# Kernel tuning notes

Measured on AMD Instinct MI355X. Metric: run time of the kernel, lower is better.

Reference implementation:

```python
import jax, jax.numpy as jnp
import numpy as np

B, P, E = 16, 1024, 768
HID, HEADS = 768, 12
DH = HID // HEADS  # 64
EPS = 1e-5


def setup_inputs() -> dict:
    key = jax.random.key(0)
    ks = jax.random.split(key, 4)
    return {
        "x": jax.random.normal(ks[0], (B, P, E), dtype=jnp.float32),
        "ln_weight": jnp.ones((P, E), dtype=jnp.float32),
        "ln_bias": jnp.zeros((P, E), dtype=jnp.float32),
        "qkv": jax.random.normal(ks[1], (E, 3 * HID), dtype=jnp.float32),
        "lin_w": jax.random.normal(ks[2], (HID, E), dtype=jnp.float32) * 0.02,
        "lin_b": jax.random.normal(ks[3], (E,), dtype=jnp.float32) * 0.02,
    }


def reference(x, ln_weight, ln_bias, qkv, lin_w, lin_b):
    # LayerNorm over the last TWO dims (patches, emb), per torch nn.LayerNorm((P, E))
    mean = jnp.mean(x, axis=(-2, -1), keepdims=True)
    var = jnp.var(x, axis=(-2, -1), keepdims=True)
    xn = (x - mean) / jnp.sqrt(var + EPS) * ln_weight + ln_bias

    # QKV projection: [B,P,E] @ [E,3*HID] -> [B,P,3*HID]
    proj = xn @ qkv
    # view(B,P,heads,-1) then permute -> [B,heads,P,3*DH]; chunk along last dim
    proj = proj.reshape(B, P, HEADS, 3 * DH).transpose(0, 2, 1, 3)
    q, k, v = proj[..., :DH], proj[..., DH:2 * DH], proj[..., 2 * DH:]

    # Softmax-free attention: (Q K^T) V
    atten = jnp.einsum("bhqd,bhkd->bhqk", q, k)  # [B,H,P,P]
    out = jnp.einsum("bhqk,bhkd->bhqd", atten, v)  # [B,H,P,DH]

    out = out.transpose(0, 2, 1, 3).reshape(B, P, HID)
    # dropout p=0.0 (eval) -> identity
    out = jax.nn.relu(out @ lin_w + lin_b)
    return out + x
```

## Files before the change

### kernel.cpp

```cpp
#include <hip/hip_runtime.h>
#include <hip/hip_bf16.h>
#include <cstdint>

#define BB   16
#define PP   1024
#define EE   768
#define HID  768
#define NH   12
#define DH   64
#define NPB  (PP * EE)
#define MROWS (BB * PP)

typedef __bf16 bf16_t;
typedef __bf16 bf16x8 __attribute__((ext_vector_type(8)));
typedef float  f32x4  __attribute__((ext_vector_type(4)));

__device__ __forceinline__ void gld16(const void* g, void* l) {
    __builtin_amdgcn_global_load_lds(
        (const __attribute__((address_space(1))) void*)(uintptr_t)g,
        (__attribute__((address_space(3))) void*)(uint32_t)(uintptr_t)l,
        16, 0, 0);
}

__global__ __launch_bounds__(256) void stats1_kernel(const float* __restrict__ x,
                                                     float* __restrict__ part) {
    int bid = blockIdx.x;
    int b = bid >> 6, s = bid & 63;
    const float4* xp = (const float4*)(x + (size_t)b * NPB + (size_t)s * 12288);
    float sum = 0.f, ss = 0.f;
#pragma unroll
    for (int i = 0; i < 12; ++i) {
        float4 v = xp[i * 256 + threadIdx.x];
        sum += v.x + v.y + v.z + v.w;
        ss  += v.x * v.x + v.y * v.y + v.z * v.z + v.w * v.w;
    }
#pragma unroll
    for (int off = 32; off > 0; off >>= 1) {
        sum += __shfl_down(sum, off, 64);
        ss  += __shfl_down(ss,  off, 64);
    }
    __shared__ float tmp[8];
    int wave = threadIdx.x >> 6, lane = threadIdx.x & 63;
    if (lane == 0) { tmp[wave * 2] = sum; tmp[wave * 2 + 1] = ss; }
    __syncthreads();
    if (threadIdx.x == 0) {
        part[bid * 2]     = tmp[0] + tmp[2] + tmp[4] + tmp[6];
        part[bid * 2 + 1] = tmp[1] + tmp[3] + tmp[5] + tmp[7];
    }
}

__global__ __launch_bounds__(256) void prep_kernel(const float* __restrict__ qkvw,
                                                   const float* __restrict__ linw,
                                                   const float* __restrict__ part,
                                                   bf16_t* __restrict__ qkvT,
                                                   bf16_t* __restrict__ lwT,
                                                   float* __restrict__ stats) {
    int bid = blockIdx.x;
    if (bid < 576) {
        __shared__ float lds[64][65];
        const float* src; bf16_t* dst; int r0, c0, W;
        if (bid < 432) {
            int tr = bid / 36, tc = bid - tr * 36;
            r0 = tr * 64; c0 = tc * 64; src = qkvw; W = 2304; dst = qkvT;
        } else {
            int bb = bid - 432;
            int tr = bb / 12, tc = bb - tr * 12;
            r0 = tr * 64; c0 = tc * 64; src = linw; W = 768; dst = lwT;
        }
        int t = threadIdx.x;
        int rr = t >> 4, cc4 = (t & 15) * 4;
#pragma unroll
        for (int j = 0; j < 4; ++j) {
            float4 v = *(const float4*)(src + (size_t)(r0 + rr + j * 16) * W + c0 + cc4);
            lds[rr + j * 16][cc4 + 0] = v.x;
            lds[rr + j * 16][cc4 + 1] = v.y;
            lds[rr + j * 16][cc4 + 2] = v.z;
            lds[rr + j * 16][cc4 + 3] = v.w;
        }
        __syncthreads();
        int cl = t >> 3, rgl = (t & 7) * 8;
#pragma unroll
        for (int jj = 0; jj < 2; ++jj) {
            int c = jj * 32 + cl;
            union { bf16_t h[8]; uint4 u; } o;
#pragma unroll
            for (int k = 0; k < 8; ++k) o.h[k] = (bf16_t)lds[rgl + k][c];
            *(uint4*)(dst + (size_t)(c0 + c) * 768 + r0 + rgl) = o.u;
        }
    } else {
        int wave = threadIdx.x >> 6, lane = threadIdx.x & 63;
#pragma unroll
        for (int j = 0; j < 4; ++j) {
            int b = wave * 4 + j;
            float sum = part[(b * 64 + lane) * 2];
            float ss  = part[(b * 64 + lane) * 2 + 1];
#pragma unroll
            for (int off = 32; off > 0; off >>= 1) {
                sum += __shfl_down(sum, off, 64);
                ss  += __shfl_down(ss,  off, 64);
            }
            if (lane == 0) {
                const float inv_n = 1.f / (float)NPB;
                float mean = sum * inv_n;
                float var  = ss * inv_n - mean * mean;
                stats[b * 2]     = mean;
                stats[b * 2 + 1] = rsqrtf(var + 1e-5f);
            }
        }
    }
}

__global__ __launch_bounds__(256) void ln_apply_kernel(const float* __restrict__ x,
                                                       const float* __restrict__ lnw,
                                                       const float* __restrict__ lnb,
                                                       const float* __restrict__ stats,
                                                       bf16_t* __restrict__ xn) {
    int i = (blockIdx.x * 256 + threadIdx.x) * 8;
    int b = i / NPB;
    int r = i - b * NPB;
    float mean = stats[b * 2], rstd = stats[b * 2 + 1];
    float4 x0 = *(const float4*)(x + i),     x1 = *(const float4*)(x + i + 4);
    float4 w0 = *(const float4*)(lnw + r),   w1 = *(const float4*)(lnw + r + 4);
    float4 c0 = *(const float4*)(lnb + r),   c1 = *(const float4*)(lnb + r + 4);
    union { bf16_t h[8]; uint4 u; } o;
    o.h[0] = (bf16_t)((x0.x - mean) * rstd * w0.x + c0.x);
    o.h[1] = (bf16_t)((x0.y - mean) * rstd * w0.y + c0.y);
    o.h[2] = (bf16_t)((x0.z - mean) * rstd * w0.z + c0.z);
    o.h[3] = (bf16_t)((x0.w - mean) * rstd * w0.w + c0.w);
    o.h[4] = (bf16_t)((x1.x - mean) * rstd * w1.x + c1.x);
    o.h[5] = (bf16_t)((x1.y - mean) * rstd * w1.y + c1.y);
    o.h[6] = (bf16_t)((x1.z - mean) * rstd * w1.z + c1.z);
    o.h[7] = (bf16_t)((x1.w - mean) * rstd * w1.w + c1.w);
    *(uint4*)(xn + i) = o.u;
}

template <int KDIM>
__device__ __forceinline__ void gemm_core_128(const bf16_t* __restrict__ A,
                                              const bf16_t* __restrict__ Bt,
                                              int mBase, int nBase,
                                              f32x4 acc[4][4],
                                              bf16_t* As, bf16_t* Bs) {
    const int t = threadIdx.x;
    const int lane = t & 63, wave = t >> 6;
    const int wm = wave >> 1, wn = wave & 1;
    const int m16 = lane & 15, quad = lane >> 4;

    const int sr = t >> 3, s8 = t & 7;
    const bf16_t* pa[4]; const bf16_t* pb[4];
#pragma unroll
    for (int i = 0; i < 4; ++i) {
        int row = i * 32 + sr;
        int g = (s8 - (row & 7)) & 7;
        pa[i] = A  + (size_t)(mBase + row) * KDIM + g * 8;
        pb[i] = Bt + (size_t)(nBase + row) * KDIM + g * 8;
    }

    int raOff[4][2], rbOff[4][2];
#pragma unroll
    for (int i = 0; i < 4; ++i) {
        int ra = wm * 64 + i * 16 + m16;
        int rb = wn * 64 + i * 16 + m16;
#pragma unroll
        for (int ks = 0; ks < 2; ++ks) {
            raOff[i][ks] = ra * 64 + (((ks * 4 + quad) + (ra & 7)) & 7) * 8;
            rbOff[i][ks] = rb * 64 + (((ks * 4 + quad) + (rb & 7)) & 7) * 8;
        }
    }

    const f32x4 z = {0.f, 0.f, 0.f, 0.f};
#pragma unroll
    for (int mm = 0; mm < 4; ++mm)
#pragma unroll
        for (int nn = 0; nn < 4; ++nn) acc[mm][nn] = z;

    for (int k0 = 0; k0 < KDIM; k0 += 64) {
        __syncthreads();
#pragma unroll
        for (int i = 0; i < 4; ++i) {
            gld16(pa[i] + k0, As + i * 2048 + t * 8);
            gld16(pb[i] + k0, Bs + i * 2048 + t * 8);
        }
        __syncthreads();
#pragma unroll
        for (int ks = 0; ks < 2; ++ks) {
            bf16x8 af[4], bfv[4];
#pragma unroll
            for (int i = 0; i < 4; ++i) {
                af[i]  = *(const bf16x8*)(As + raOff[i][ks]);
                bfv[i] = *(const bf16x8*)(Bs + rbOff[i][ks]);
            }
#pragma unroll
            for (int mm = 0; mm < 4; ++mm)
#pragma unroll
                for (int nn = 0; nn < 4; ++nn)
                    acc[mm][nn] = __builtin_amdgcn_mfma_f32_16x16x32_bf16(
                        af[mm], bfv[nn], acc[mm][nn], 0, 0, 0);
        }
    }
}

__global__ __launch_bounds__(256, 2) void gemm_qkv_kernel(const bf16_t* __restrict__ xn,
                                                          const bf16_t* __restrict__ qkvT,
                                                          bf16_t* __restrict__ q,
                                                          bf16_t* __restrict__ kt,
                                                          bf16_t* __restrict__ vt) {
    __shared__ bf16_t smem[24576];
    const int t = threadIdx.x, lane = t & 63, wave = t >> 6;
    const int wm = wave >> 1, wn = wave & 1;
    const int m16 = lane & 15, quad = lane >> 4;

    const int lb = blockIdx.y * 9 + blockIdx.x;
    const int id = (lb & 7) * 144 + (lb >> 3);
    const int tx = id % 9, ty = id / 9;
    const int mBase = ty * 128, nBase = tx * 256;

    const bf16_t* gsrc[6];
    int ldst[6];
#pragma unroll
    for (int j = 0; j < 2; ++j) {
        int c = t + 256 * j;
        int l = c >> 3, lg = ((c & 7) - (l & 7)) & 7;
        gsrc[j] = xn + (size_t)(mBase + l + (lg >> 2) * 64) * 768 + (lg & 3) * 8;
        ldst[j] = c * 8;
    }
#pragma unroll
    for (int j = 0; j < 4; ++j) {
        int c = t + 256 * j;
        int l = c >> 3, lg = ((c & 7) - (l & 7)) & 7;
        gsrc[2 + j] = qkvT + (size_t)(nBase + l + (lg >> 2) * 128) * 768 + (lg & 3) * 8;
        ldst[2 + j] = 4096 + c * 8;
    }

    int aOff[4], bOff[8];
#pragma unroll
    for (int mf = 0; mf < 4; ++mf)
        aOff[mf] = (mf * 16 + m16) * 64 + (((wm * 4 + quad) + (m16 & 7)) & 7) * 8;
#pragma unroll
    for (int nf = 0; nf < 8; ++nf)
        bOff[nf] = 4096 + (nf * 16 + m16) * 64 + (((wn * 4 + quad) + (m16 & 7)) & 7) * 8;

    f32x4 acc[4][8];
    const f32x4 z = {0.f, 0.f, 0.f, 0.f};
#pragma unroll
    for (int mf = 0; mf < 4; ++mf)
#pragma unroll
        for (int nf = 0; nf < 8; ++nf) acc[mf][nf] = z;

#pragma unroll
    for (int j = 0; j < 6; ++j) gld16(gsrc[j], smem + ldst[j]);
    __syncthreads();

#pragma unroll
    for (int it = 0; it < 12; ++it) {
#pragma unroll
        for (int s = 0; s < 2; ++s) {
            const int step = it * 2 + s;
            const int par = s * 12288, nxt = 12288 - par;
            if (step < 23) {
                const int kq = (step + 1) * 32;
#pragma unroll
                for (int j = 0; j < 6; ++j)
                    gld16(gsrc[j] + kq, smem + nxt + ldst[j]);
            }
            bf16x8 af[4], bf0[4], bf1[4];
#pragma unroll
            for (int mf = 0; mf < 4; ++mf)
                af[mf] = *(const bf16x8*)(smem + par + aOff[mf]);
#pragma unroll
            for (int nf = 0; nf < 4; ++nf)
                bf0[nf] = *(const bf16x8*)(smem + par + bOff[nf]);
            __builtin_amdgcn_s_setprio(1);
#pragma unroll
            for (int mf = 0; mf < 4; ++mf)
#pragma unroll
                for (int nf = 0; nf < 4; ++nf)
                    acc[mf][nf] = __builtin_amdgcn_mfma_f32_16x16x32_bf16(
                        af[mf], bf0[nf], acc[mf][nf], 0, 0, 0);
            __builtin_amdgcn_s_setprio(0);
            __builtin_amdgcn_s_barrier();
#pragma unroll
            for (int nf = 0; nf < 4; ++nf)
                bf1[nf] = *(const bf16x8*)(smem + par + bOff[4 + nf]);
            __builtin_amdgcn_s_setprio(1);
#pragma unroll
            for (int mf = 0; mf < 4; ++mf)
#pragma unroll
                for (int nf = 0; nf < 4; ++nf)
                    acc[mf][4 + nf] = __builtin_amdgcn_mfma_f32_16x16x32_bf16(
                        af[mf], bf1[nf], acc[mf][4 + nf], 0, 0, 0);
            __builtin_amdgcn_s_setprio(0);
            __syncthreads();
        }
    }

    bf16_t* slot = smem + wave * 4608;
    const int b = mBase >> 10, p0 = mBase & 1023;

#pragma unroll
    for (int half = 0; half < 2; ++half) {
        const int g64 = tx * 4 + wn * 2 + half;
        const int cls = g64 % 3, h = g64 / 3;
        if (cls == 0) {
#pragma unroll
            for (int mf = 0; mf < 4; ++mf)
#pragma unroll
                for (int nfl = 0; nfl < 4; ++nfl)
#pragma unroll
                    for (int i = 0; i < 4; ++i)
                        slot[(mf * 16 + quad * 4 + i) * 72 + nfl * 16 + m16] =
                            (bf16_t)acc[mf][half * 4 + nfl][i];
            asm volatile("s_waitcnt lgkmcnt(0)" ::: "memory");
            __builtin_amdgcn_sched_barrier(0);
#pragma unroll
            for (int j = 0; j < 8; ++j) {
                int r = j * 8 + (lane >> 3), cc = lane & 7;
                bf16x8 val = *(const bf16x8*)(slot + r * 72 + cc * 8);
                *(bf16x8*)(q + ((size_t)(b * 1024 + p0 + wm * 64 + r)) * 768 +
                           h * 64 + cc * 8) = val;
            }
        } else {
            bf16_t* dst = (cls == 1) ? kt : vt;
            const size_t bh = (size_t)(b * 12 + h);
#pragma unroll
            for (int mf = 0; mf < 4; ++mf)
#pragma unroll
                for (int nfl = 0; nfl < 4; ++nfl) {
                    int c = nfl * 16 + m16;
                    union { bf16_t hh[4]; uint2 u; } pk;
#pragma unroll
                    for (int i = 0; i < 4; ++i)
                        pk.hh[i] = (bf16_t)acc[mf][half * 4 + nfl][i];
                    *(uint2*)(slot + c * 72 + mf * 16 + quad * 4) = pk.u;
                }
            asm volatile("s_waitcnt lgkmcnt(0)" ::: "memory");
            __builtin_amdgcn_sched_barrier(0);
#pragma unroll
            for (int j = 0; j < 8; ++j) {
                int c = (lane >> 3) + j * 8, r8 = (lane & 7) * 8;
                bf16x8 val = *(const bf16x8*)(slot + c * 72 + r8);
                *(bf16x8*)(dst + (bh * 64 + c) * 1024 + p0 + wm * 64 + r8) = val;
            }
        }
        if (half == 0) {
            asm volatile("s_waitcnt lgkmcnt(0)" ::: "memory");
            __builtin_amdgcn_sched_barrier(0);
        }
    }
}

__global__ __launch_bounds__(256) void kv_kernel(const bf16_t* __restrict__ kt,
                                                 const bf16_t* __restrict__ vt,
                                                 bf16_t* __restrict__ thi,
                                                 bf16_t* __restrict__ tlo) {
    __shared__ float red[4 * 64 * 65];
    const int bh = blockIdx.x;
    const bf16_t* Kb = kt + (size_t)bh * DH * PP;
    const bf16_t* Vb = vt + (size_t)bh * DH * PP;
    const int t = threadIdx.x;
    const int lane = t & 63, wave = t >> 6;
    const int m16 = lane & 15, quad = lane >> 4;
    const f32x4 z = {0.f, 0.f, 0.f, 0.f};
    f32x4 acc[4][4];
#pragma unroll
    for (int mm = 0; mm < 4; ++mm)
#pragma unroll
        for (int nn = 0; nn < 4; ++nn) acc[mm][nn] = z;

    for (int ks = 0; ks < 8; ++ks) {
        int kb = wave * 256 + ks * 32 + quad * 8;
        bf16x8 af[4], bfv[4];
#pragma unroll
        for (int mm = 0; mm < 4; ++mm)
            af[mm] = *(const bf16x8*)(Kb + (size_t)(mm * 16 + m16) * PP + kb);
#pragma unroll
        for (int nn = 0; nn < 4; ++nn)
            bfv[nn] = *(const bf16x8*)(Vb + (size_t)(nn * 16 + m16) * PP + kb);
#pragma unroll
        for (int mm = 0; mm < 4; ++mm)
#pragma unroll
            for (int nn = 0; nn < 4; ++nn)
                acc[mm][nn] = __builtin_amdgcn_mfma_f32_16x16x32_bf16(
                    af[mm], bfv[nn], acc[mm][nn], 0, 0, 0);
    }
#pragma unroll
    for (int mm = 0; mm < 4; ++mm)
#pragma unroll
        for (int nn = 0; nn < 4; ++nn)
#pragma unroll
            for (int i = 0; i < 4; ++i)
                red[wave * 4160 + (mm * 16 + quad * 4 + i) * 65 + nn * 16 + m16] =
                    acc[mm][nn][i];
    __syncthreads();
#pragma unroll
    for (int j = 0; j < 16; ++j) {
        int idx = j * 256 + t;
        int m = idx >> 6, n = idx & 63;
        int a = m * 65 + n;
        float s = red[a] + red[4160 + a] + red[8320 + a] + red[12480 + a];
        bf16_t hi = (bf16_t)s;
        float lo = s - (float)hi;
        thi[(size_t)bh * 4096 + idx] = hi;
        tlo[(size_t)bh * 4096 + idx] = (bf16_t)lo;
    }
}

__global__ __launch_bounds__(256) void u_kernel(const bf16_t* __restrict__ thi,
                                                const bf16_t* __restrict__ tlo,
                                                const bf16_t* __restrict__ lwT,
                                                bf16_t* __restrict__ ut) {
    const int bh = blockIdx.x;
    const int b = bh / NH, h = bh - b * NH;
    const int nBase = blockIdx.y * 256;
    const bf16_t* Th = thi + (size_t)bh * 4096;
    const bf16_t* Tl = tlo + (size_t)bh * 4096;
    const int t = threadIdx.x, lane = t & 63, wave = t >> 6;
    const int wm = wave >> 1, wn = wave & 1;
    const int m16 = lane & 15, quad = lane >> 4;
    const f32x4 z = {0.f, 0.f, 0.f, 0.f};
    f32x4 acc[2][8];
#pragma unroll
    for (int mm = 0; mm < 2; ++mm)
#pragma unroll
        for (int nn = 0; nn < 8; ++nn) acc[mm][nn] = z;

#pragma unroll
    for (int ks = 0; ks < 2; ++ks) {
        bf16x8 ah[2], al[2], bfr[8];
#pragma unroll
        for (int mm = 0; mm < 2; ++mm) {
            ah[mm] = *(const bf16x8*)(Th + (wm * 32 + mm * 16 + m16) * 64 + ks * 32 + quad * 8);
            al[mm] = *(const bf16x8*)(Tl + (wm * 32 + mm * 16 + m16) * 64 + ks * 32 + quad * 8);
        }
#pragma unroll
        for (int nn = 0; nn < 8; ++nn)
            bfr[nn] = *(const bf16x8*)(
                lwT + (size_t)(nBase + wn * 128 + nn * 16 + m16) * 768 + h * 64 + ks * 32 + quad * 8);
#pragma unroll
        for (int mm = 0; mm < 2; ++mm)
#pragma unroll
            for (int nn = 0; nn < 8; ++nn) {
                acc[mm][nn] = __builtin_amdgcn_mfma_f32_16x16x32_bf16(
                    ah[mm], bfr[nn], acc[mm][nn], 0, 0, 0);
                acc[mm][nn] = __builtin_amdgcn_mfma_f32_16x16x32_bf16(
                    al[mm], bfr[nn], acc[mm][nn], 0, 0, 0);
            }
    }
#pragma unroll
    for (int mm = 0; mm < 2; ++mm)
#pragma unroll
        for (int nn = 0; nn < 8; ++nn) {
            int e  = nBase + wn * 128 + nn * 16 + m16;
            int d1 = wm * 32 + mm * 16 + quad * 4;
            union { bf16_t hh[4]; uint2 u; } pk;
#pragma unroll
            for (int i = 0; i < 4; ++i) pk.hh[i] = (bf16_t)acc[mm][nn][i];
            *(uint2*)(ut + ((size_t)b * 768 + e) * 768 + h * 64 + d1) = pk.u;
        }
}

__global__ __launch_bounds__(256) void gemm_out_kernel(const bf16_t* __restrict__ q,
                                                       const bf16_t* __restrict__ ut,
                                                       const float* __restrict__ linb,
                                                       const float* __restrict__ x,
                                                       float* __restrict__ out) {
    __shared__ bf16_t smem[16384];
    f32x4 acc[4][4];
    const int lb  = blockIdx.y * 6 + blockIdx.x;
    const int swz = (lb & 7) * 96 + (lb >> 3);
    const int tx  = swz % 6, ty = swz / 6;
    const int mBase = ty * 128, nBase = tx * 128;
    const int b = mBase >> 10;
    gemm_core_128<768>(q, ut + (size_t)b * 768 * 768, mBase, nBase, acc,
                       smem, smem + 8192);

    const int lane = threadIdx.x & 63, wave = threadIdx.x >> 6;
    const int wm = wave >> 1, wn = wave & 1;
    const int m16 = lane & 15, quad = lane >> 4;
#pragma unroll
    for (int mm = 0; mm < 4; ++mm) {
#pragma unroll
        for (int i = 0; i < 4; ++i) {
            size_t row = mBase + wm * 64 + mm * 16 + quad * 4 + i;
#pragma unroll
            for (int nn = 0; nn < 4; ++nn) {
                int col = nBase + wn * 64 + nn * 16 + m16;
                float v = acc[mm][nn][i] + linb[col];
                v = fmaxf(v, 0.f) + x[row * EE + col];
                out[row * EE + col] = v;
            }
        }
    }
}

extern "C" void kernel_launch(void* const* d_in, const int* in_sizes, int n_in,
                              void* d_out, int out_size, void* d_ws, size_t ws_size,
                              hipStream_t stream) {
    const float* x    = (const float*)d_in[0];
    const float* lnw  = (const float*)d_in[1];
    const float* lnb  = (const float*)d_in[2];
    const float* qkvw = (const float*)d_in[3];
    const float* linw = (const float*)d_in[4];
    const float* linb = (const float*)d_in[5];
    float* out = (float*)d_out;
    char* ws = (char*)d_ws;

    float*  part  = (float*)(ws + 0);
    float*  stats = (float*)(ws + 8192);
    bf16_t* xn    = (bf16_t*)(ws + 8448);
    bf16_t* qkvT  = (bf16_t*)(ws + 25174272);
    bf16_t* lwT   = (bf16_t*)(ws + 28713216);
    bf16_t* q     = (bf16_t*)(ws + 29892864);
    bf16_t* kt    = (bf16_t*)(ws + 55058688);
    bf16_t* vt    = (bf16_t*)(ws + 80224512);
    bf16_t* thi   = qkvT;
    bf16_t* tlo   = qkvT + 192 * 4096;
    bf16_t* ut    = kt;

    stats1_kernel<<<dim3(BB * 64), dim3(256), 0, stream>>>(x, part);
    prep_kernel<<<dim3(577), dim3(256), 0, stream>>>(qkvw, linw, part, qkvT, lwT, stats);
    ln_apply_kernel<<<dim3(6144), dim3(256), 0, stream>>>(x, lnw, lnb, stats, xn);
    gemm_qkv_kernel<<<dim3(9, 128), dim3(256), 0, stream>>>(xn, qkvT, q, kt, vt);
    kv_kernel<<<dim3(192), dim3(256), 0, stream>>>(kt, vt, thi, tlo);
    u_kernel<<<dim3(192, 3), dim3(256), 0, stream>>>(thi, tlo, lwT, ut);
    gemm_out_kernel<<<dim3(6, 128), dim3(256), 0, stream>>>(q, ut, linb, x, out);
}
```

Baseline: 261.0 us.

## Triple-buffer QKV GEMM LDS pipeline with prefetch distance two

```diff
diff --git a/kernel.cpp b/kernel.cpp
--- a/kernel.cpp
+++ b/kernel.cpp
@@ -204,7 +204,7 @@
                                                           bf16_t* __restrict__ q,
                                                           bf16_t* __restrict__ kt,
                                                           bf16_t* __restrict__ vt) {
-    __shared__ bf16_t smem[24576];
+    __shared__ bf16_t smem[36864];
     const int t = threadIdx.x, lane = t & 63, wave = t >> 6;
     const int wm = wave >> 1, wn = wave & 1;
     const int m16 = lane & 15, quad = lane >> 4;
@@ -248,51 +248,59 @@
 
 #pragma unroll
     for (int j = 0; j < 6; ++j) gld16(gsrc[j], smem + ldst[j]);
-    __syncthreads();
-
-#pragma unroll
-    for (int it = 0; it < 12; ++it) {
-#pragma unroll
-        for (int s = 0; s < 2; ++s) {
-            const int step = it * 2 + s;
-            const int par = s * 12288, nxt = 12288 - par;
-            if (step < 23) {
-                const int kq = (step + 1) * 32;
-#pragma unroll
-                for (int j = 0; j < 6; ++j)
-                    gld16(gsrc[j] + kq, smem + nxt + ldst[j]);
-            }
-            bf16x8 af[4], bf0[4], bf1[4];
-#pragma unroll
-            for (int mf = 0; mf < 4; ++mf)
-                af[mf] = *(const bf16x8*)(smem + par + aOff[mf]);
+#pragma unroll
+    for (int j = 0; j < 6; ++j) gld16(gsrc[j] + 32, smem + 12288 + ldst[j]);
+
+#pragma unroll
+    for (int step = 0; step < 24; ++step) {
+        const int cur = (step % 3) * 12288;
+        asm volatile("s_waitcnt lgkmcnt(0)" ::: "memory");
+        __builtin_amdgcn_sched_barrier(0);
+        __builtin_amdgcn_s_barrier();
+        if (step + 2 < 24) {
+            const int nb = ((step + 2) % 3) * 12288;
+            const int kq = (step + 2) * 32;
+#pragma unroll
+            for (int j = 0; j < 6; ++j)
+                gld16(gsrc[j] + kq, smem + nb + ldst[j]);
+        }
+        if (step < 22)       asm volatile("s_waitcnt vmcnt(12)" ::: "memory");
+        else if (step == 22) asm volatile("s_waitcnt vmcnt(6)"  ::: "memory");
+        else                 asm volatile("s_waitcnt vmcnt(0)"  ::: "memory");
+        __builtin_amdgcn_sched_barrier(0);
+        __builtin_amdgcn_s_barrier();
+
+        bf16x8 af[4], bf0[4], bf1[4];
+#pragma unroll
+        for (int mf = 0; mf < 4; ++mf)
+            af[mf] = *(const bf16x8*)(smem + cur + aOff[mf]);
+#pragma unroll
+        for (int nf = 0; nf < 4; ++nf)
+            bf0[nf] = *(const bf16x8*)(smem + cur + bOff[nf]);
+        __builtin_amdgcn_s_setprio(1);
+#pragma unroll
+        for (int mf = 0; mf < 4; ++mf)
 #pragma unroll
             for (int nf = 0; nf < 4; ++nf)
-                bf0[nf] = *(const bf16x8*)(smem + par + bOff[nf]);
-            __builtin_amdgcn_s_setprio(1);
-#pragma unroll
-            for (int mf = 0; mf < 4; ++mf)
-#pragma unroll
-                for (int nf = 0; nf < 4; ++nf)
-                    acc[mf][nf] = __builtin_amdgcn_mfma_f32_16x16x32_bf16(
-                        af[mf], bf0[nf], acc[mf][nf], 0, 0, 0);
-            __builtin_amdgcn_s_setprio(0);
-            __builtin_amdgcn_s_barrier();
+                acc[mf][nf] = __builtin_amdgcn_mfma_f32_16x16x32_bf16(
+                    af[mf], bf0[nf], acc[mf][nf], 0, 0, 0);
+        __builtin_amdgcn_s_setprio(0);
+        __builtin_amdgcn_s_barrier();
+#pragma unroll
+        for (int nf = 0; nf < 4; ++nf)
+            bf1[nf] = *(const bf16x8*)(smem + cur + bOff[4 + nf]);
+        __builtin_amdgcn_s_setprio(1);
+#pragma unroll
+        for (int mf = 0; mf < 4; ++mf)
 #pragma unroll
             for (int nf = 0; nf < 4; ++nf)
-                bf1[nf] = *(const bf16x8*)(smem + par + bOff[4 + nf]);
-            __builtin_amdgcn_s_setprio(1);
-#pragma unroll
-            for (int mf = 0; mf < 4; ++mf)
-#pragma unroll
-                for (int nf = 0; nf < 4; ++nf)
-                    acc[mf][4 + nf] = __builtin_amdgcn_mfma_f32_16x16x32_bf16(
-                        af[mf], bf1[nf], acc[mf][4 + nf], 0, 0, 0);
-            __builtin_amdgcn_s_setprio(0);
-            __syncthreads();
-        }
-    }
-
+                acc[mf][4 + nf] = __builtin_amdgcn_mfma_f32_16x16x32_bf16(
+                    af[mf], bf1[nf], acc[mf][4 + nf], 0, 0, 0);
+        __builtin_amdgcn_s_setprio(0);
+    }
+
+    asm volatile("s_waitcnt lgkmcnt(0)" ::: "memory");
+    __builtin_amdgcn_sched_barrier(0);
     bf16_t* slot = smem + wave * 4608;
     const int b = mBase >> 10, p0 = mBase & 1023;
 
```

After: 257.1 us. About the same (-1.5%).
